# Kernel optimization log

Hardware: AMD Instinct MI355X
Metric: run time of the kernel (lower is better)

## Reference

```python
import jax, jax.numpy as jnp
import numpy as np


def setup_inputs() -> dict:
    key = jax.random.key(0)
    k1, k2 = jax.random.split(key)
    context_emb = jax.random.normal(k1, (8, 2048, 768), dtype=jnp.float32)
    query_emb = jax.random.normal(k2, (8, 512, 768), dtype=jnp.float32)
    return {"context_emb": context_emb, "query_emb": query_emb}


def reference(context_emb, query_emb):
    # temp[b, q, c] = sum_d query[b,q,d] * context[b,c,d]
    temp = jnp.einsum("bqd,bcd->bqc", query_emb, context_emb)
    # softmax over the query axis (dim=1 in torch)
    alpha = jax.nn.softmax(temp, axis=1)  # [B, Lq, Lc]
    # attention_weighted_query[b, c, d] = sum_q query[b,q,d] * alpha[b,q,c]
    awq = jnp.einsum("bqd,bqc->bcd", query_emb, alpha)  # [B, Lc, D]
    # elementwise gate against context
    return context_emb * awq
```

## Files before the change

kernel.cpp:

```cpp
#include <hip/hip_runtime.h>

#define NB 8
#define LQ 512
#define LC 2048
#define DD 768

typedef _Float16 f16x8 __attribute__((ext_vector_type(8)));
typedef _Float16 f16x4 __attribute__((ext_vector_type(4)));
typedef float    f32x4 __attribute__((ext_vector_type(4)));

__global__ __launch_bounds__(256) void preconvert_q(const float* __restrict__ Q,
                                                    _Float16* __restrict__ Qh,
                                                    _Float16* __restrict__ QhT) {
    __shared__ _Float16 lt[64][68];
    const int blk = blockIdx.x;
    const int b   = blk / 96;
    const int rem = blk % 96;
    const int q0  = (rem / 12) * 64;
    const int d0  = (rem % 12) * 64;
    const int t   = threadIdx.x;
    const int tr  = t >> 4;
    const int tc  = t & 15;

    const float* Qb  = Q  + ((size_t)b * LQ + q0) * DD + d0;
    _Float16*    Qhb = Qh + ((size_t)b * LQ + q0) * DD + d0;

#pragma unroll
    for (int i = 0; i < 4; i++) {
        const int row = i * 16 + tr;
        const int col = tc * 4;
        f32x4 v = *(const f32x4*)(Qb + (size_t)row * DD + col);
        f16x4 h;
        h.x = (_Float16)v.x; h.y = (_Float16)v.y;
        h.z = (_Float16)v.z; h.w = (_Float16)v.w;
        *(f16x4*)(Qhb + (size_t)row * DD + col) = h;
        *(f16x4*)&lt[row][col] = h;
    }
    __syncthreads();

    _Float16* QTb = QhT + ((size_t)b * DD + d0) * LQ + q0;
#pragma unroll
    for (int i = 0; i < 4; i++) {
        const int drow = i * 16 + tr;
        const int qc   = tc * 4;
        f16x4 h;
        h.x = lt[qc + 0][drow];
        h.y = lt[qc + 1][drow];
        h.z = lt[qc + 2][drow];
        h.w = lt[qc + 3][drow];
        *(f16x4*)(QTb + (size_t)drow * LQ + qc) = h;
    }
}

#define CM        64
#define A_SLOTS   96
#define P_SLOTS   64
#define RED_OFF   65536
#define BBUF_OFF  98304
#define CBUF_OFF  65536
#define SMEM_BYTES 163840

__device__ __forceinline__ void dma16(const _Float16* g, char* l) {
    __builtin_amdgcn_global_load_lds(
        (const __attribute__((address_space(1))) unsigned int*)g,
        (__attribute__((address_space(3))) unsigned int*)l,
        16, 0, 0);
}

__global__ __launch_bounds__(512, 2) void gated_attn(const float* __restrict__ ctx,
                                                     const _Float16* __restrict__ Qh,
                                                     const _Float16* __restrict__ QhT,
                                                     float* __restrict__ out) {
    __shared__ __align__(16) char smem[SMEM_BYTES];
    float (*red_max)[64] = (float (*)[64])(smem + RED_OFF);
    float (*red_sum)[64] = (float (*)[64])(smem + RED_OFF + 2048);

    const int b    = blockIdx.x & 7;
    const int c0   = (blockIdx.x >> 3) * CM;
    const int t    = threadIdx.x;
    const int w    = t >> 6;
    const int lane = t & 63;
    const int quad = lane >> 4;
    const int l15  = lane & 15;

    const float*    Cb  = ctx + ((size_t)b * LC + c0) * DD;
    const _Float16* Qhb = Qh  + (size_t)b * LQ * DD;
    const _Float16* QTb = QhT + (size_t)b * DD * LQ;

    const int srow = t >> 2;
    const int sse  = (t & 3) ^ (srow & 3) ^ ((srow >> 2) & 3);
    const _Float16* stA = Qhb + (size_t)srow * DD + sse * 8;
    const _Float16* stC = QTb + (size_t)srow * LQ + sse * 8;
    char* ldsW = smem + (size_t)w * 1024;

    const int bsub = ((quad ^ (l15 & 3) ^ ((l15 >> 2) & 3)) & 3) * 16;

#pragma unroll
    for (int j = 0; j < 4; j++)
        dma16(stA + (size_t)(j * 128) * DD, ldsW + BBUF_OFF + j * 8192);

#pragma unroll
    for (int i = 0; i < 12; i++) {
        const int idx = i * 512 + t;
        const int row = idx / 96;
        const int c16 = idx % 96;
        const float* p = Cb + (size_t)row * DD + c16 * 8;
        f32x4 f0 = *(const f32x4*)p;
        f32x4 f1 = *(const f32x4*)(p + 4);
        f16x8 v;
        v[0] = (_Float16)f0.x; v[1] = (_Float16)f0.y;
        v[2] = (_Float16)f0.z; v[3] = (_Float16)f0.w;
        v[4] = (_Float16)f1.x; v[5] = (_Float16)f1.y;
        v[6] = (_Float16)f1.z; v[7] = (_Float16)f1.w;
        const int s16 = row * A_SLOTS + ((c16 & ~7) | ((c16 ^ row) & 7));
        *(f16x8*)(smem + (size_t)s16 * 16) = v;
    }
    __syncthreads();

    f32x4 acc[4][4];
#pragma unroll
    for (int mt = 0; mt < 4; mt++)
#pragma unroll
        for (int nt = 0; nt < 4; nt++)
            acc[mt][nt] = (f32x4){0.f, 0.f, 0.f, 0.f};

#pragma unroll
    for (int kc = 0; kc < 24; kc++) {
        if (kc > 0) __syncthreads();
        if (kc + 1 < 24) {
            char* nb = ldsW + BBUF_OFF + ((kc + 1) & 1) * 32768;
            const _Float16* src = stA + (kc + 1) * 32;
#pragma unroll
            for (int j = 0; j < 4; j++)
                dma16(src + (size_t)(j * 128) * DD, nb + j * 8192);
        }
        const char* bbuf = smem + BBUF_OFF + (kc & 1) * 32768;
        const int c16 = kc * 4 + quad;
        const int sw  = (c16 & ~7) | ((c16 ^ l15) & 7);
        f16x8 a[4], bq[4];
#pragma unroll
        for (int mt = 0; mt < 4; mt++)
            a[mt] = *(const f16x8*)(smem + (size_t)((mt * 16 + l15) * A_SLOTS + sw) * 16);
#pragma unroll
        for (int nt = 0; nt < 4; nt++)
            bq[nt] = *(const f16x8*)(bbuf + (size_t)(w * 64 + nt * 16 + l15) * 64 + bsub);
        __builtin_amdgcn_s_setprio(1);
#pragma unroll
        for (int nt = 0; nt < 4; nt++)
#pragma unroll
            for (int mt = 0; mt < 4; mt++)
                acc[mt][nt] = __builtin_amdgcn_mfma_f32_16x16x32_f16(a[mt], bq[nt], acc[mt][nt], 0, 0, 0);
        __builtin_amdgcn_s_setprio(0);
    }

    float rm[4][4];
#pragma unroll
    for (int mt = 0; mt < 4; mt++)
#pragma unroll
        for (int r = 0; r < 4; r++)
            rm[mt][r] = -1e30f;
#pragma unroll
    for (int mt = 0; mt < 4; mt++)
#pragma unroll
        for (int nt = 0; nt < 4; nt++) {
            rm[mt][0] = fmaxf(rm[mt][0], acc[mt][nt].x);
            rm[mt][1] = fmaxf(rm[mt][1], acc[mt][nt].y);
            rm[mt][2] = fmaxf(rm[mt][2], acc[mt][nt].z);
            rm[mt][3] = fmaxf(rm[mt][3], acc[mt][nt].w);
        }
#pragma unroll
    for (int off = 1; off < 16; off <<= 1)
#pragma unroll
        for (int mt = 0; mt < 4; mt++)
#pragma unroll
            for (int r = 0; r < 4; r++)
                rm[mt][r] = fmaxf(rm[mt][r], __shfl_xor(rm[mt][r], off));
    if (l15 == 0) {
#pragma unroll
        for (int mt = 0; mt < 4; mt++)
#pragma unroll
            for (int r = 0; r < 4; r++)
                red_max[w][mt * 16 + quad * 4 + r] = rm[mt][r];
    }
    __syncthreads();

    float fm[4][4];
#pragma unroll
    for (int mt = 0; mt < 4; mt++)
#pragma unroll
        for (int r = 0; r < 4; r++) {
            const int row = mt * 16 + quad * 4 + r;
            float m0 = fmaxf(fmaxf(red_max[0][row], red_max[1][row]),
                             fmaxf(red_max[2][row], red_max[3][row]));
            float m1 = fmaxf(fmaxf(red_max[4][row], red_max[5][row]),
                             fmaxf(red_max[6][row], red_max[7][row]));
            fm[mt][r] = fmaxf(m0, m1);
        }
    float rs[4][4];
#pragma unroll
    for (int mt = 0; mt < 4; mt++)
#pragma unroll
        for (int r = 0; r < 4; r++)
            rs[mt][r] = 0.f;
#pragma unroll
    for (int mt = 0; mt < 4; mt++)
#pragma unroll
        for (int nt = 0; nt < 4; nt++) {
            float e0 = __expf(acc[mt][nt].x - fm[mt][0]);
            float e1 = __expf(acc[mt][nt].y - fm[mt][1]);
            float e2 = __expf(acc[mt][nt].z - fm[mt][2]);
            float e3 = __expf(acc[mt][nt].w - fm[mt][3]);
            acc[mt][nt].x = e0; acc[mt][nt].y = e1;
            acc[mt][nt].z = e2; acc[mt][nt].w = e3;
            rs[mt][0] += e0; rs[mt][1] += e1; rs[mt][2] += e2; rs[mt][3] += e3;
        }
#pragma unroll
    for (int off = 1; off < 16; off <<= 1)
#pragma unroll
        for (int mt = 0; mt < 4; mt++)
#pragma unroll
            for (int r = 0; r < 4; r++)
                rs[mt][r] += __shfl_xor(rs[mt][r], off);
    if (l15 == 0) {
#pragma unroll
        for (int mt = 0; mt < 4; mt++)
#pragma unroll
            for (int r = 0; r < 4; r++)
                red_sum[w][mt * 16 + quad * 4 + r] = rs[mt][r];
    }
    __syncthreads();

#pragma unroll
    for (int mt = 0; mt < 4; mt++)
#pragma unroll
        for (int r = 0; r < 4; r++) {
            const int row = mt * 16 + quad * 4 + r;
            float s = 0.f;
#pragma unroll
            for (int j = 0; j < 8; j++) s += red_sum[j][row];
            const float inv = 1.0f / s;
#pragma unroll
            for (int nt = 0; nt < 4; nt++) {
                acc[mt][nt].x = (r == 0) ? acc[mt][nt].x * inv : acc[mt][nt].x;
                acc[mt][nt].y = (r == 1) ? acc[mt][nt].y * inv : acc[mt][nt].y;
                acc[mt][nt].z = (r == 2) ? acc[mt][nt].z * inv : acc[mt][nt].z;
                acc[mt][nt].w = (r == 3) ? acc[mt][nt].w * inv : acc[mt][nt].w;
            }
        }
    __syncthreads();

#pragma unroll
    for (int j = 0; j < 6; j++)
        dma16(stC + (size_t)(j * 128) * LQ, ldsW + CBUF_OFF + j * 8192);

#pragma unroll
    for (int mt = 0; mt < 4; mt++)
#pragma unroll
        for (int r = 0; r < 4; r++) {
            const int row = mt * 16 + quad * 4 + r;
#pragma unroll
            for (int nt = 0; nt < 4; nt++) {
                const int q = w * 64 + nt * 16 + l15;
                float v = (r == 0 ? acc[mt][nt].x : r == 1 ? acc[mt][nt].y
                          : r == 2 ? acc[mt][nt].z : acc[mt][nt].w);
                const int c16 = q >> 3;
                const int s16 = row * P_SLOTS + ((c16 & ~7) | ((c16 ^ row) & 7));
                *(_Float16*)(smem + (size_t)s16 * 16 + (q & 7) * 2) = (_Float16)v;
            }
        }
    __syncthreads();

    f32x4 acc2[4][6];
#pragma unroll
    for (int mt = 0; mt < 4; mt++)
#pragma unroll
        for (int nt = 0; nt < 6; nt++)
            acc2[mt][nt] = (f32x4){0.f, 0.f, 0.f, 0.f};

#pragma unroll
    for (int kc = 0; kc < 16; kc++) {
        if (kc > 0) __syncthreads();
        if (kc + 1 < 16) {
            char* nb = ldsW + CBUF_OFF + ((kc + 1) & 1) * 49152;
            const _Float16* src = stC + (kc + 1) * 32;
#pragma unroll
            for (int j = 0; j < 6; j++)
                dma16(src + (size_t)(j * 128) * LQ, nb + j * 8192);
        }
        const char* cbuf = smem + CBUF_OFF + (kc & 1) * 49152;
        const int c16 = kc * 4 + quad;
        const int sw  = (c16 & ~7) | ((c16 ^ l15) & 7);
        f16x8 pf[4], cq[6];
#pragma unroll
        for (int mt = 0; mt < 4; mt++)
            pf[mt] = *(const f16x8*)(smem + (size_t)((mt * 16 + l15) * P_SLOTS + sw) * 16);
#pragma unroll
        for (int nt = 0; nt < 6; nt++)
            cq[nt] = *(const f16x8*)(cbuf + (size_t)(w * 96 + nt * 16 + l15) * 64 + bsub);
        __builtin_amdgcn_s_setprio(1);
#pragma unroll
        for (int nt = 0; nt < 6; nt++)
#pragma unroll
            for (int mt = 0; mt < 4; mt++)
                acc2[mt][nt] = __builtin_amdgcn_mfma_f32_16x16x32_f16(pf[mt], cq[nt], acc2[mt][nt], 0, 0, 0);
        __builtin_amdgcn_s_setprio(0);
    }

#pragma unroll
    for (int mt = 0; mt < 4; mt++)
#pragma unroll
        for (int nt = 0; nt < 6; nt++) {
            const int col = w * 96 + nt * 16 + l15;
#pragma unroll
            for (int r = 0; r < 4; r++) {
                const int rl  = mt * 16 + quad * 4 + r;
                const size_t idx = ((size_t)b * LC + c0 + rl) * DD + col;
                float v = (r == 0 ? acc2[mt][nt].x : r == 1 ? acc2[mt][nt].y
                          : r == 2 ? acc2[mt][nt].z : acc2[mt][nt].w);
                out[idx] = ctx[idx] * v;
            }
        }
}

extern "C" void kernel_launch(void* const* d_in, const int* in_sizes, int n_in,
                              void* d_out, int out_size, void* d_ws, size_t ws_size,
                              hipStream_t stream) {
    const float* ctx = (const float*)d_in[0];
    const float* q   = (const float*)d_in[1];
    float* out = (float*)d_out;

    const size_t nQ = (size_t)NB * LQ * DD;
    _Float16* Qh  = (_Float16*)d_ws;
    _Float16* QhT = Qh + nQ;

    preconvert_q<<<dim3(NB * 96), dim3(256), 0, stream>>>(q, Qh, QhT);
    gated_attn<<<dim3(NB * (LC / CM)), dim3(512), 0, stream>>>(ctx, Qh, QhT, out);
}
```

Baseline: 151.8 us.

## Split fused attention into QK-softmax and PV-gate kernels via fp16 P workspace

Splits the single fused kernel in two. The first computes QK^T plus the softmax over the query axis and writes normalized fp16 probabilities to a global workspace. It now streams context chunks through double-buffered LDS instead of staging the whole 64x768 tile up front, which cuts LDS use enough for 4 blocks per CU. The second kernel does a tiled P·Q GEMM over 128x128 output tiles plus the context gate, launching more blocks with less LDS each to raise occupancy and parallelism. The cost is an extra launch and a global round trip for the 8x2048x512 fp16 P matrix.

```diff
diff --git a/kernel.cpp b/kernel.cpp
--- a/kernel.cpp
+++ b/kernel.cpp
@@ -8,6 +8,13 @@
 typedef _Float16 f16x8 __attribute__((ext_vector_type(8)));
 typedef _Float16 f16x4 __attribute__((ext_vector_type(4)));
 typedef float    f32x4 __attribute__((ext_vector_type(4)));
+
+__device__ __forceinline__ void dma16(const _Float16* g, char* l) {
+    __builtin_amdgcn_global_load_lds(
+        (const __attribute__((address_space(1))) unsigned int*)g,
+        (__attribute__((address_space(3))) unsigned int*)l,
+        16, 0, 0);
+}
 
 __global__ __launch_bounds__(256) void preconvert_q(const float* __restrict__ Q,
                                                     _Float16* __restrict__ Qh,
@@ -52,70 +59,56 @@
     }
 }
 
-#define CM        64
-#define A_SLOTS   96
-#define P_SLOTS   64
-#define RED_OFF   65536
-#define BBUF_OFF  98304
-#define CBUF_OFF  65536
-#define SMEM_BYTES 163840
-
-__device__ __forceinline__ void dma16(const _Float16* g, char* l) {
-    __builtin_amdgcn_global_load_lds(
-        (const __attribute__((address_space(1))) unsigned int*)g,
-        (__attribute__((address_space(3))) unsigned int*)l,
-        16, 0, 0);
-}
-
-__global__ __launch_bounds__(512, 2) void gated_attn(const float* __restrict__ ctx,
+
+#define K1_B0   0
+#define K1_B1   32768
+#define K1_A0   65536
+#define K1_A1   69632
+#define K1_RMAX 73728
+#define K1_RSUM 75776
+#define K1_SMEM 77824
+
+__global__ __launch_bounds__(512, 4) void qk_softmax(const float* __restrict__ ctx,
                                                      const _Float16* __restrict__ Qh,
-                                                     const _Float16* __restrict__ QhT,
-                                                     float* __restrict__ out) {
-    __shared__ __align__(16) char smem[SMEM_BYTES];
-    float (*red_max)[64] = (float (*)[64])(smem + RED_OFF);
-    float (*red_sum)[64] = (float (*)[64])(smem + RED_OFF + 2048);
+                                                     _Float16* __restrict__ P) {
+    __shared__ __align__(16) char smem[K1_SMEM];
+    float (*red_max)[64] = (float (*)[64])(smem + K1_RMAX);
+    float (*red_sum)[64] = (float (*)[64])(smem + K1_RSUM);
 
     const int b    = blockIdx.x & 7;
-    const int c0   = (blockIdx.x >> 3) * CM;
+    const int c0   = (blockIdx.x >> 3) * 64;
     const int t    = threadIdx.x;
     const int w    = t >> 6;
     const int lane = t & 63;
     const int quad = lane >> 4;
     const int l15  = lane & 15;
 
-    const float*    Cb  = ctx + ((size_t)b * LC + c0) * DD;
-    const _Float16* Qhb = Qh  + (size_t)b * LQ * DD;
-    const _Float16* QTb = QhT + (size_t)b * DD * LQ;
+    const _Float16* QhB = Qh + (size_t)b * LQ * DD;
 
     const int srow = t >> 2;
-    const int sse  = (t & 3) ^ (srow & 3) ^ ((srow >> 2) & 3);
-    const _Float16* stA = Qhb + (size_t)srow * DD + sse * 8;
-    const _Float16* stC = QTb + (size_t)srow * LQ + sse * 8;
-    char* ldsW = smem + (size_t)w * 1024;
-
-    const int bsub = ((quad ^ (l15 & 3) ^ ((l15 >> 2) & 3)) & 3) * 16;
+    const int sB   = (t & 3) ^ (srow & 3) ^ ((srow >> 2) & 3);
+    const _Float16* stB = QhB + (size_t)srow * DD + sB * 8;
+    char* dmaW = smem + (size_t)w * 1024;
+
+    const int arow = t >> 3;
+    const int ags  = (t & 7) >> 1;
+    const int ah   = t & 1;
+    const int asw  = ags ^ (arow & 3) ^ ((arow >> 2) & 3);
+    const float* ctxA = ctx + ((size_t)b * LC + c0 + arow) * DD + asw * 8 + ah * 4;
+    const int aWoff = arow * 64 + ags * 16 + ah * 8;
+
+    const int fl   = (l15 & 3) ^ ((l15 >> 2) & 3);
+    const int bsub = (quad ^ fl) * 16;
 
 #pragma unroll
     for (int j = 0; j < 4; j++)
-        dma16(stA + (size_t)(j * 128) * DD, ldsW + BBUF_OFF + j * 8192);
-
-#pragma unroll
-    for (int i = 0; i < 12; i++) {
-        const int idx = i * 512 + t;
-        const int row = idx / 96;
-        const int c16 = idx % 96;
-        const float* p = Cb + (size_t)row * DD + c16 * 8;
-        f32x4 f0 = *(const f32x4*)p;
-        f32x4 f1 = *(const f32x4*)(p + 4);
-        f16x8 v;
-        v[0] = (_Float16)f0.x; v[1] = (_Float16)f0.y;
-        v[2] = (_Float16)f0.z; v[3] = (_Float16)f0.w;
-        v[4] = (_Float16)f1.x; v[5] = (_Float16)f1.y;
-        v[6] = (_Float16)f1.z; v[7] = (_Float16)f1.w;
-        const int s16 = row * A_SLOTS + ((c16 & ~7) | ((c16 ^ row) & 7));
-        *(f16x8*)(smem + (size_t)s16 * 16) = v;
-    }
-    __syncthreads();
+        dma16(stB + (size_t)(j * 128) * DD, dmaW + K1_B0 + j * 8192);
+    {
+        f32x4 v = *(const f32x4*)ctxA;
+        f16x4 h; h.x = (_Float16)v.x; h.y = (_Float16)v.y;
+        h.z = (_Float16)v.z; h.w = (_Float16)v.w;
+        *(f16x4*)(smem + K1_A0 + aWoff) = h;
+    }
 
     f32x4 acc[4][4];
 #pragma unroll
@@ -126,24 +119,29 @@
 
 #pragma unroll
     for (int kc = 0; kc < 24; kc++) {
-        if (kc > 0) __syncthreads();
+        __syncthreads();
+        f16x4 aS;
         if (kc + 1 < 24) {
-            char* nb = ldsW + BBUF_OFF + ((kc + 1) & 1) * 32768;
-            const _Float16* src = stA + (kc + 1) * 32;
+            char* nb = dmaW + (((kc + 1) & 1) ? K1_B1 : K1_B0);
+            const _Float16* src = stB + (kc + 1) * 32;
 #pragma unroll
             for (int j = 0; j < 4; j++)
                 dma16(src + (size_t)(j * 128) * DD, nb + j * 8192);
-        }
-        const char* bbuf = smem + BBUF_OFF + (kc & 1) * 32768;
-        const int c16 = kc * 4 + quad;
-        const int sw  = (c16 & ~7) | ((c16 ^ l15) & 7);
+            f32x4 v = *(const f32x4*)(ctxA + (kc + 1) * 32);
+            aS.x = (_Float16)v.x; aS.y = (_Float16)v.y;
+            aS.z = (_Float16)v.z; aS.w = (_Float16)v.w;
+        }
+        const char* bbuf = smem + ((kc & 1) ? K1_B1 : K1_B0);
+        const char* abuf = smem + ((kc & 1) ? K1_A1 : K1_A0);
         f16x8 a[4], bq[4];
 #pragma unroll
         for (int mt = 0; mt < 4; mt++)
-            a[mt] = *(const f16x8*)(smem + (size_t)((mt * 16 + l15) * A_SLOTS + sw) * 16);
+            a[mt] = *(const f16x8*)(abuf + (size_t)(mt * 16 + l15) * 64 + bsub);
 #pragma unroll
         for (int nt = 0; nt < 4; nt++)
             bq[nt] = *(const f16x8*)(bbuf + (size_t)(w * 64 + nt * 16 + l15) * 64 + bsub);
+        if (kc + 1 < 24)
+            *(f16x4*)(smem + (((kc + 1) & 1) ? K1_A1 : K1_A0) + aWoff) = aS;
         __builtin_amdgcn_s_setprio(1);
 #pragma unroll
         for (int nt = 0; nt < 4; nt++)
@@ -230,6 +228,7 @@
     }
     __syncthreads();
 
+    _Float16* Pb = P + ((size_t)b * LC + c0) * LQ;
 #pragma unroll
     for (int mt = 0; mt < 4; mt++)
 #pragma unroll
@@ -239,84 +238,104 @@
 #pragma unroll
             for (int j = 0; j < 8; j++) s += red_sum[j][row];
             const float inv = 1.0f / s;
-#pragma unroll
-            for (int nt = 0; nt < 4; nt++) {
-                acc[mt][nt].x = (r == 0) ? acc[mt][nt].x * inv : acc[mt][nt].x;
-                acc[mt][nt].y = (r == 1) ? acc[mt][nt].y * inv : acc[mt][nt].y;
-                acc[mt][nt].z = (r == 2) ? acc[mt][nt].z * inv : acc[mt][nt].z;
-                acc[mt][nt].w = (r == 3) ? acc[mt][nt].w * inv : acc[mt][nt].w;
-            }
-        }
-    __syncthreads();
-
-#pragma unroll
-    for (int j = 0; j < 6; j++)
-        dma16(stC + (size_t)(j * 128) * LQ, ldsW + CBUF_OFF + j * 8192);
-
-#pragma unroll
-    for (int mt = 0; mt < 4; mt++)
-#pragma unroll
-        for (int r = 0; r < 4; r++) {
-            const int row = mt * 16 + quad * 4 + r;
 #pragma unroll
             for (int nt = 0; nt < 4; nt++) {
                 const int q = w * 64 + nt * 16 + l15;
                 float v = (r == 0 ? acc[mt][nt].x : r == 1 ? acc[mt][nt].y
                           : r == 2 ? acc[mt][nt].z : acc[mt][nt].w);
-                const int c16 = q >> 3;
-                const int s16 = row * P_SLOTS + ((c16 & ~7) | ((c16 ^ row) & 7));
-                *(_Float16*)(smem + (size_t)s16 * 16 + (q & 7) * 2) = (_Float16)v;
+                Pb[(size_t)row * LQ + q] = (_Float16)(v * inv);
             }
         }
-    __syncthreads();
-
-    f32x4 acc2[4][6];
-#pragma unroll
-    for (int mt = 0; mt < 4; mt++)
-#pragma unroll
-        for (int nt = 0; nt < 6; nt++)
-            acc2[mt][nt] = (f32x4){0.f, 0.f, 0.f, 0.f};
+}
+
+#define K2_A0 0
+#define K2_A1 8192
+#define K2_B0 16384
+#define K2_B1 24576
+#define K2_SMEM 32768
+
+__global__ __launch_bounds__(256, 4) void pv_gate(const float* __restrict__ ctx,
+                                                  const _Float16* __restrict__ P,
+                                                  const _Float16* __restrict__ QhT,
+                                                  float* __restrict__ out) {
+    __shared__ __align__(16) char smem[K2_SMEM];
+
+    const int b    = blockIdx.x & 7;
+    const int r8   = blockIdx.x >> 3;
+    const int c0   = (r8 % 16) * 128;
+    const int d0   = (r8 / 16) * 128;
+    const int t    = threadIdx.x;
+    const int w    = t >> 6;
+    const int lane = t & 63;
+    const int quad = lane >> 4;
+    const int l15  = lane & 15;
+    const int wr   = w >> 1;
+    const int wc   = w & 1;
+
+    const int srow = t >> 2;
+    const int sS   = (t & 3) ^ (srow & 3) ^ ((srow >> 2) & 3);
+    const _Float16* stA = P   + ((size_t)b * LC + c0 + srow) * LQ + sS * 8;
+    const _Float16* stB = QhT + ((size_t)b * DD + d0 + srow) * LQ + sS * 8;
+    char* dmaW = smem + (size_t)w * 1024;
+
+    const int fl   = (l15 & 3) ^ ((l15 >> 2) & 3);
+    const int bsub = (quad ^ fl) * 16;
+
+#pragma unroll
+    for (int j = 0; j < 2; j++) {
+        dma16(stA + (size_t)(j * 64) * LQ, dmaW + K2_A0 + j * 4096);
+        dma16(stB + (size_t)(j * 64) * LQ, dmaW + K2_B0 + j * 4096);
+    }
+
+    f32x4 acc[4][4];
+#pragma unroll
+    for (int mt = 0; mt < 4; mt++)
+#pragma unroll
+        for (int nt = 0; nt < 4; nt++)
+            acc[mt][nt] = (f32x4){0.f, 0.f, 0.f, 0.f};
 
 #pragma unroll
     for (int kc = 0; kc < 16; kc++) {
-        if (kc > 0) __syncthreads();
+        __syncthreads();
         if (kc + 1 < 16) {
-            char* nb = ldsW + CBUF_OFF + ((kc + 1) & 1) * 49152;
-            const _Float16* src = stC + (kc + 1) * 32;
-#pragma unroll
-            for (int j = 0; j < 6; j++)
-                dma16(src + (size_t)(j * 128) * LQ, nb + j * 8192);
-        }
-        const char* cbuf = smem + CBUF_OFF + (kc & 1) * 49152;
-        const int c16 = kc * 4 + quad;
-        const int sw  = (c16 & ~7) | ((c16 ^ l15) & 7);
-        f16x8 pf[4], cq[6];
-#pragma unroll
-        for (int mt = 0; mt < 4; mt++)
-            pf[mt] = *(const f16x8*)(smem + (size_t)((mt * 16 + l15) * P_SLOTS + sw) * 16);
-#pragma unroll
-        for (int nt = 0; nt < 6; nt++)
-            cq[nt] = *(const f16x8*)(cbuf + (size_t)(w * 96 + nt * 16 + l15) * 64 + bsub);
+            const int nb = ((kc + 1) & 1);
+            const _Float16* sa = stA + (kc + 1) * 32;
+            const _Float16* sb = stB + (kc + 1) * 32;
+#pragma unroll
+            for (int j = 0; j < 2; j++) {
+                dma16(sa + (size_t)(j * 64) * LQ, dmaW + (nb ? K2_A1 : K2_A0) + j * 4096);
+                dma16(sb + (size_t)(j * 64) * LQ, dmaW + (nb ? K2_B1 : K2_B0) + j * 4096);
+            }
+        }
+        const char* abuf = smem + ((kc & 1) ? K2_A1 : K2_A0);
+        const char* bbuf = smem + ((kc & 1) ? K2_B1 : K2_B0);
+        f16x8 a[4], bq[4];
+#pragma unroll
+        for (int mt = 0; mt < 4; mt++)
+            a[mt] = *(const f16x8*)(abuf + (size_t)(wr * 64 + mt * 16 + l15) * 64 + bsub);
+#pragma unroll
+        for (int nt = 0; nt < 4; nt++)
+            bq[nt] = *(const f16x8*)(bbuf + (size_t)(wc * 64 + nt * 16 + l15) * 64 + bsub);
         __builtin_amdgcn_s_setprio(1);
 #pragma unroll
-        for (int nt = 0; nt < 6; nt++)
+        for (int nt = 0; nt < 4; nt++)
 #pragma unroll
             for (int mt = 0; mt < 4; mt++)
-                acc2[mt][nt] = __builtin_amdgcn_mfma_f32_16x16x32_f16(pf[mt], cq[nt], acc2[mt][nt], 0, 0, 0);
+                acc[mt][nt] = __builtin_amdgcn_mfma_f32_16x16x32_f16(a[mt], bq[nt], acc[mt][nt], 0, 0, 0);
         __builtin_amdgcn_s_setprio(0);
     }
 
 #pragma unroll
     for (int mt = 0; mt < 4; mt++)
 #pragma unroll
-        for (int nt = 0; nt < 6; nt++) {
-            const int col = w * 96 + nt * 16 + l15;
+        for (int nt = 0; nt < 4; nt++) {
+            const int col = d0 + wc * 64 + nt * 16 + l15;
 #pragma unroll
             for (int r = 0; r < 4; r++) {
-                const int rl  = mt * 16 + quad * 4 + r;
-                const size_t idx = ((size_t)b * LC + c0 + rl) * DD + col;
-                float v = (r == 0 ? acc2[mt][nt].x : r == 1 ? acc2[mt][nt].y
-                          : r == 2 ? acc2[mt][nt].z : acc2[mt][nt].w);
+                const int row = c0 + wr * 64 + mt * 16 + quad * 4 + r;
+                const size_t idx = ((size_t)b * LC + row) * DD + col;
+                float v = (r == 0 ? acc[mt][nt].x : r == 1 ? acc[mt][nt].y
+                          : r == 2 ? acc[mt][nt].z : acc[mt][nt].w);
                 out[idx] = ctx[idx] * v;
             }
         }
@@ -332,7 +351,9 @@
     const size_t nQ = (size_t)NB * LQ * DD;
     _Float16* Qh  = (_Float16*)d_ws;
     _Float16* QhT = Qh + nQ;
+    _Float16* Pws = QhT + nQ;
 
     preconvert_q<<<dim3(NB * 96), dim3(256), 0, stream>>>(q, Qh, QhT);
-    gated_attn<<<dim3(NB * (LC / CM)), dim3(512), 0, stream>>>(ctx, Qh, QhT, out);
-}
+    qk_softmax<<<dim3(NB * (LC / 64)), dim3(512), 0, stream>>>(ctx, Qh, Pws);
+    pv_gate<<<dim3(NB * (LC / 128) * (DD / 128)), dim3(256), 0, stream>>>(ctx, Pws, QhT, out);
+}
```

After: 158.7 us. 1.05x slower.
